# Kernel optimization log

Measured on AMD Instinct MI355X. Metric: run time of the kernel, lower is better.

Reference implementation:

```python
import jax, jax.numpy as jnp
import numpy as np

IN_CH, C_M, C_N = 512, 512, 128
B, H, W = 16, 56, 56


def setup_inputs() -> dict:
    key = jax.random.key(0)
    ks = jax.random.split(key, 7)
    s = 1.0 / np.sqrt(IN_CH)
    return {
        "x": jax.random.normal(ks[0], (B, IN_CH, H, W), dtype=jnp.float32),
        "wA": jax.random.uniform(ks[1], (C_M, IN_CH), jnp.float32, -s, s),
        "bA": jax.random.uniform(ks[2], (C_M,), jnp.float32, -s, s),
        "wB": jax.random.uniform(ks[3], (C_N, IN_CH), jnp.float32, -s, s),
        "bB": jax.random.uniform(ks[4], (C_N,), jnp.float32, -s, s),
        "wV": jax.random.uniform(ks[5], (C_N, IN_CH), jnp.float32, -s, s),
        "bV": jax.random.uniform(ks[6], (C_N,), jnp.float32, -s, s),
        "K": 1,
    }


def reference(x, wA, bA, wB, bB, wV, bV, K):
    b, c, h, w = x.shape
    c_m, c_n = wA.shape[0], wB.shape[0]
    batch = b // K
    hw = h * w
    N = K * hw
    # 1x1 convs == channel-wise matmuls
    A = jnp.einsum('bchw,mc->bmhw', x, wA) + bA[None, :, None, None]
    Bf = jnp.einsum('bchw,nc->bnhw', x, wB) + bB[None, :, None, None]
    Vf = jnp.einsum('bchw,nc->bnhw', x, wV) + bV[None, :, None, None]
    # (batch, c_m, K*h*w)
    tmpA = A.reshape(batch, K, c_m, hw).transpose(0, 2, 1, 3).reshape(batch, c_m, N)
    # softmax over the spatial dim N (torch Softmax() on 2D -> dim=1)
    tmpB = Bf.reshape(batch, K, c_n, hw).transpose(0, 2, 1, 3).reshape(batch, c_n, N)
    attB = jax.nn.softmax(tmpB, axis=-1).transpose(0, 2, 1)  # (batch, N, c_n)
    # softmax over channel dim c_n
    tmpV = Vf.reshape(batch, K, c_n, hw).transpose(0, 1, 3, 2).reshape(batch, N, c_n)
    attV = jax.nn.softmax(tmpV, axis=-1).transpose(0, 2, 1)  # (batch, c_n, N)
    G = jnp.matmul(tmpA, attB)   # (batch, c_m, c_n) global descriptors
    Z = jnp.matmul(G, attV)      # (batch, c_m, N) distribute
    Z = Z.reshape(batch, c_m, K, hw).transpose(0, 2, 1, 3).reshape(b, c_m, h, w)
    return Z
```

## Files before the change

kernel.cpp:

```cpp
#include <hip/hip_runtime.h>
#include <hip/hip_bf16.h>

#define BATCH 16
#define CIN   512
#define HW    3136
#define CM    512
#define CN    128

typedef short short8 __attribute__((ext_vector_type(8)));
typedef float f32x4  __attribute__((ext_vector_type(4)));

#define MFMA(a,b,c) __builtin_amdgcn_mfma_f32_16x16x32_bf16((a),(b),(c),0,0,0)

__device__ __forceinline__ void cvt_store8(__bf16* dst, const float* src) {
  const f32x4 a = *(const f32x4*)src;
  const f32x4 b = *(const f32x4*)(src + 4);
  __attribute__((aligned(16))) __bf16 t[8];
  t[0] = (__bf16)a[0]; t[1] = (__bf16)a[1]; t[2] = (__bf16)a[2]; t[3] = (__bf16)a[3];
  t[4] = (__bf16)b[0]; t[5] = (__bf16)b[1]; t[6] = (__bf16)b[2]; t[7] = (__bf16)b[3];
  *(uint4*)dst = *(uint4*)t;
}

__device__ __forceinline__ void load_lds16(const void* g, void* l) {
  __builtin_amdgcn_global_load_lds(
      (const __attribute__((address_space(1))) unsigned int*)g,
      (__attribute__((address_space(3))) unsigned int*)l, 16, 0, 0);
}

__global__ __launch_bounds__(256) void prep_w_kernel(
    const float* __restrict__ wB, const float* __restrict__ wV,
    __bf16* __restrict__ Wimg)
{
  const int k0  = blockIdx.x >> 2;
  const int row = (blockIdx.x & 3) * 64 + (threadIdx.x >> 2);
  const int c0  = (threadIdx.x & 3) * 16;
  const float* src = (row < 128) ? (wB + (size_t)row * CIN)
                                 : (wV + (size_t)(row - 128) * CIN);
  src += k0 * 64 + c0;
  __bf16* dst = Wimg + (size_t)k0 * 18432 + row * 72 + c0;
  cvt_store8(dst, src);
  cvt_store8(dst + 8, src + 8);
}

__global__ __launch_bounds__(256) void conv_bv_kernel(
    const float* __restrict__ x,
    const __bf16* __restrict__ Wimg,
    const float* __restrict__ bB, const float* __restrict__ bV,
    __bf16* __restrict__ BVB, __bf16* __restrict__ attVT,
    float* __restrict__ bsum)
{
  const int s0  = blockIdx.x * 64;
  const int b   = blockIdx.y;
  const int tid = threadIdx.x;
  const int lane = tid & 63, w = tid >> 6;
  const int l15  = lane & 15, q = lane >> 4;

  __shared__ __attribute__((aligned(16))) char smem[46080];
  __bf16* Wt = (__bf16*)smem;
  __bf16* Xt = (__bf16*)(smem + 36864);
  __bf16* T  = (__bf16*)smem;
  __shared__ float Vm[2][64];
  __shared__ float Vs[2][64];

  f32x4 acc[4][4] = {};
  const float* xb = x + (size_t)b*CIN*HW + s0;
  const int colg = tid & 7;
  const int cl = 2*(tid >> 3);
  const int xoff = ((cl >> 3) ^ colg)*8 + (cl & 7);

  f32x4 pa0, pa1, pb0, pb1;
  {
    const float* r0 = xb + (size_t)cl*HW + colg*8;
    const float* r1 = r0 + HW;
    pa0 = *(const f32x4*)r0; pa1 = *(const f32x4*)(r0 + 4);
    pb0 = *(const f32x4*)r1; pb1 = *(const f32x4*)(r1 + 4);
  }

  for (int k0 = 0; k0 < CIN; k0 += 64) {
    {
      float va[8] = {pa0[0],pa0[1],pa0[2],pa0[3],pa1[0],pa1[1],pa1[2],pa1[3]};
      float vb[8] = {pb0[0],pb0[1],pb0[2],pb0[3],pb1[0],pb1[1],pb1[2],pb1[3]};
      #pragma unroll
      for (int j = 0; j < 8; ++j) {
        int s = colg*8 + j;
        __attribute__((aligned(4))) __bf16 pairv[2] = { (__bf16)va[j], (__bf16)vb[j] };
        *(unsigned int*)&Xt[s*72 + xoff] = *(unsigned int*)pairv;
      }
    }
    {
      const char* wsrc = (const char*)Wimg + (size_t)(k0 >> 6)*36864 + tid*16;
      char* wdst = (char*)Wt + tid*16;
      #pragma unroll
      for (int i = 0; i < 9; ++i)
        load_lds16(wsrc + i*4096, wdst + i*4096);
    }
    if (k0 + 64 < CIN) {
      const float* r0 = xb + (size_t)(k0 + 64 + cl)*HW + colg*8;
      const float* r1 = r0 + HW;
      pa0 = *(const f32x4*)r0; pa1 = *(const f32x4*)(r0 + 4);
      pb0 = *(const f32x4*)r1; pb1 = *(const f32x4*)(r1 + 4);
    }
    __syncthreads();
    #pragma unroll
    for (int kk = 0; kk < 2; ++kk) {
      short8 a[4], bb[4];
      #pragma unroll
      for (int mi = 0; mi < 4; ++mi)
        a[mi] = *(short8*)&Wt[(w*64 + mi*16 + l15)*72 + kk*32 + q*8];
      #pragma unroll
      for (int si = 0; si < 4; ++si) {
        int s = si*16 + l15;
        int oct = (kk*4 + q) ^ (si*2 + (l15 >> 3));
        bb[si] = *(short8*)&Xt[s*72 + oct*8];
      }
      #pragma unroll
      for (int mi = 0; mi < 4; ++mi)
        #pragma unroll
        for (int si = 0; si < 4; ++si)
          acc[mi][si] = MFMA(a[mi], bb[si], acc[mi][si]);
    }
    __syncthreads();
  }

  float bias[4][4];
  #pragma unroll
  for (int mi = 0; mi < 4; ++mi)
    #pragma unroll
    for (int r = 0; r < 4; ++r) {
      int nch = w*64 + mi*16 + q*4 + r;
      bias[mi][r] = (nch < CN) ? bB[nch] : bV[nch - CN];
    }

  if (w < 2) {
    const size_t outb = (size_t)b * CN * HW;
    float psum[4][4] = {};
    #pragma unroll
    for (int mi = 0; mi < 4; ++mi)
      #pragma unroll
      for (int si = 0; si < 4; ++si) {
        int s = s0 + si*16 + l15;
        #pragma unroll
        for (int r = 0; r < 4; ++r) {
          int nch = w*64 + mi*16 + q*4 + r;
          __bf16 bv = (__bf16)(acc[mi][si][r] + bias[mi][r]);
          BVB[outb + (size_t)nch*HW + s] = bv;
          psum[mi][r] += __expf((float)bv);
        }
      }
    #pragma unroll
    for (int mi = 0; mi < 4; ++mi)
      #pragma unroll
      for (int r = 0; r < 4; ++r) {
        float v = psum[mi][r];
        v += __shfl_xor(v, 1); v += __shfl_xor(v, 2);
        v += __shfl_xor(v, 4); v += __shfl_xor(v, 8);
        if (l15 == 0) {
          int nch = w*64 + mi*16 + q*4 + r;
          atomicAdd(&bsum[b*CN + nch], v);
        }
      }
  } else {
    #pragma unroll
    for (int si = 0; si < 4; ++si) {
      float m = -1e30f;
      #pragma unroll
      for (int mi = 0; mi < 4; ++mi)
        #pragma unroll
        for (int r = 0; r < 4; ++r)
          m = fmaxf(m, acc[mi][si][r] + bias[mi][r]);
      m = fmaxf(m, __shfl_xor(m, 16));
      m = fmaxf(m, __shfl_xor(m, 32));
      if (q == 0) Vm[w-2][si*16 + l15] = m;
    }
  }
  __syncthreads();
  if (w >= 2) {
    #pragma unroll
    for (int si = 0; si < 4; ++si) {
      int idx = si*16 + l15;
      float ms = fmaxf(Vm[0][idx], Vm[1][idx]);
      float ssum = 0.f;
      #pragma unroll
      for (int mi = 0; mi < 4; ++mi)
        #pragma unroll
        for (int r = 0; r < 4; ++r) {
          float e = __expf(acc[mi][si][r] + bias[mi][r] - ms);
          acc[mi][si][r] = e;
          ssum += e;
        }
      ssum += __shfl_xor(ssum, 16);
      ssum += __shfl_xor(ssum, 32);
      if (q == 0) Vs[w-2][idx] = ssum;
    }
  }
  __syncthreads();
  if (w >= 2) {
    #pragma unroll
    for (int si = 0; si < 4; ++si) {
      int idx = si*16 + l15;
      float inv = 1.0f / (Vs[0][idx] + Vs[1][idx]);
      #pragma unroll
      for (int mi = 0; mi < 4; ++mi)
        #pragma unroll
        for (int r = 0; r < 4; ++r) {
          int j = (w-2)*64 + mi*16 + q*4 + r;
          T[idx*136 + j] = (__bf16)(acc[mi][si][r] * inv);
        }
    }
  }
  __syncthreads();
  __bf16* dst = attVT + ((size_t)b*HW + s0)*CN;
  #pragma unroll
  for (int k = 0; k < 4; ++k) {
    int chunk = tid + 256*k;
    int row = chunk >> 4, oct = chunk & 15;
    *(uint4*)&dst[(size_t)row*CN + oct*8] = *(uint4*)&T[row*136 + oct*8];
  }
}

__global__ __launch_bounds__(256) void h_gemm_kernel(
    const float* __restrict__ x, const __bf16* __restrict__ BVB,
    const float* __restrict__ bsum, float* __restrict__ H)
{
  const int c0 = blockIdx.x * 128, b = blockIdx.y, kc = blockIdx.z;
  const int tid = threadIdx.x, lane = tid & 63, w = tid >> 6;
  const int l15 = lane & 15, q = lane >> 4;

  __shared__ __attribute__((aligned(16))) __bf16 At[128*72];
  __shared__ __attribute__((aligned(16))) __bf16 Bt[128*72];
  f32x4 acc[8][2] = {};

  const float* xb = x + ((size_t)b*CIN + c0)*HW;
  const __bf16* ab = BVB + (size_t)b*CN*HW;
  const float* bsb = bsum + b*CN;
  const int colg = tid & 7, row0 = tid >> 3;

  float irow[4];
  #pragma unroll
  for (int p = 0; p < 4; ++p) irow[p] = 1.0f / bsb[row0 + 32*p];

  for (int ki = 0; ki < 7; ++ki) {
    int k0 = kc*448 + ki*64;
    #pragma unroll
    for (int p = 0; p < 4; ++p) {
      int row = row0 + 32*p;
      cvt_store8(&At[row*72 + colg*8], xb + (size_t)row*HW + k0 + colg*8);
    }
    #pragma unroll
    for (int p = 0; p < 4; ++p) {
      int row = row0 + 32*p;
      uint4 rawv = *(const uint4*)(ab + (size_t)row*HW + k0 + colg*8);
      const __bf16* v = (const __bf16*)&rawv;
      __attribute__((aligned(16))) __bf16 t[8];
      #pragma unroll
      for (int j = 0; j < 8; ++j)
        t[j] = (__bf16)(__expf((float)v[j]) * irow[p]);
      *(uint4*)&Bt[row*72 + colg*8] = *(uint4*)t;
    }
    __syncthreads();
    #pragma unroll
    for (int kk = 0; kk < 2; ++kk) {
      short8 a[8], bb[2];
      #pragma unroll
      for (int mi = 0; mi < 8; ++mi)
        a[mi] = *(short8*)&At[(mi*16 + l15)*72 + kk*32 + q*8];
      #pragma unroll
      for (int ni = 0; ni < 2; ++ni)
        bb[ni] = *(short8*)&Bt[(w*32 + ni*16 + l15)*72 + kk*32 + q*8];
      #pragma unroll
      for (int mi = 0; mi < 8; ++mi)
        #pragma unroll
        for (int ni = 0; ni < 2; ++ni)
          acc[mi][ni] = MFMA(a[mi], bb[ni], acc[mi][ni]);
    }
    __syncthreads();
  }

  float* Hb = H + (size_t)b*CIN*CN;
  #pragma unroll
  for (int mi = 0; mi < 8; ++mi)
    #pragma unroll
    for (int ni = 0; ni < 2; ++ni)
      #pragma unroll
      for (int r = 0; r < 4; ++r) {
        int c = c0 + mi*16 + q*4 + r;
        int n = w*32 + ni*16 + l15;
        atomicAdd(&Hb[c*CN + n], acc[mi][ni][r]);
      }
}

__global__ __launch_bounds__(256) void g_gemm_kernel(
    const float* __restrict__ wA, const float* __restrict__ bA,
    const float* __restrict__ H, __bf16* __restrict__ G)
{
  const int m0 = blockIdx.x * 64, b = blockIdx.y;
  const int tid = threadIdx.x, lane = tid & 63, w = tid >> 6;
  const int l15 = lane & 15, q = lane >> 4;

  __shared__ __attribute__((aligned(16))) __bf16 At[64*72];
  __shared__ __attribute__((aligned(16))) __bf16 Bt[128*72];
  f32x4 acc[4][2] = {};

  const float* Hb = H + (size_t)b*CIN*CN;
  const int colg = tid & 7, row0 = tid >> 3;
  const int nn = tid & 127, gh = tid >> 7;

  for (int k0 = 0; k0 < CIN; k0 += 64) {
    #pragma unroll
    for (int p = 0; p < 2; ++p) {
      int row = row0 + 32*p;
      cvt_store8(&At[row*72 + colg*8], wA + (size_t)(m0+row)*CIN + k0 + colg*8);
    }
    #pragma unroll
    for (int p = 0; p < 4; ++p) {
      int g = gh + 2*p;
      __attribute__((aligned(16))) __bf16 tmp[8];
      #pragma unroll
      for (int j = 0; j < 8; ++j)
        tmp[j] = (__bf16)Hb[(size_t)(k0 + g*8 + j)*CN + nn];
      *(uint4*)&Bt[nn*72 + g*8] = *(uint4*)tmp;
    }
    __syncthreads();
    #pragma unroll
    for (int kk = 0; kk < 2; ++kk) {
      short8 a[4], bb[2];
      #pragma unroll
      for (int mi = 0; mi < 4; ++mi)
        a[mi] = *(short8*)&At[(mi*16 + l15)*72 + kk*32 + q*8];
      #pragma unroll
      for (int ni = 0; ni < 2; ++ni)
        bb[ni] = *(short8*)&Bt[(w*32 + ni*16 + l15)*72 + kk*32 + q*8];
      #pragma unroll
      for (int mi = 0; mi < 4; ++mi)
        #pragma unroll
        for (int ni = 0; ni < 2; ++ni)
          acc[mi][ni] = MFMA(a[mi], bb[ni], acc[mi][ni]);
    }
    __syncthreads();
  }

  #pragma unroll
  for (int mi = 0; mi < 4; ++mi)
    #pragma unroll
    for (int ni = 0; ni < 2; ++ni)
      #pragma unroll
      for (int r = 0; r < 4; ++r) {
        int m = m0 + mi*16 + q*4 + r;
        int n = w*32 + ni*16 + l15;
        G[((size_t)b*CM + m)*CN + n] = (__bf16)(acc[mi][ni][r] + bA[m]);
      }
}

__global__ __launch_bounds__(256) void z_gemm_kernel(
    const __bf16* __restrict__ G, const __bf16* __restrict__ attVT,
    float* __restrict__ out)
{
  const int m0 = blockIdx.x * 128, s0 = blockIdx.y * 64, b = blockIdx.z;
  const int tid = threadIdx.x, lane = tid & 63, w = tid >> 6;
  const int l15 = lane & 15, q = lane >> 4;

  __shared__ __attribute__((aligned(16))) __bf16 At[128*136];
  __shared__ __attribute__((aligned(16))) __bf16 Bt[64*136];

  const __bf16* Gb = G + ((size_t)b*CM + m0)*CN;
  const __bf16* Vb = attVT + ((size_t)b*HW + s0)*CN;
  const int g = tid & 15, r0 = tid >> 4;
  #pragma unroll
  for (int p = 0; p < 8; ++p) {
    int row = r0 + 16*p;
    *(uint4*)&At[row*136 + g*8] = *(const uint4*)(Gb + (size_t)row*CN + g*8);
  }
  #pragma unroll
  for (int p = 0; p < 4; ++p) {
    int row = r0 + 16*p;
    *(uint4*)&Bt[row*136 + g*8] = *(const uint4*)(Vb + (size_t)row*CN + g*8);
  }
  __syncthreads();

  f32x4 acc[8] = {};
  #pragma unroll
  for (int kk = 0; kk < 4; ++kk) {
    short8 bb = *(short8*)&Bt[(w*16 + l15)*136 + kk*32 + q*8];
    #pragma unroll
    for (int mi = 0; mi < 8; ++mi) {
      short8 a = *(short8*)&At[(mi*16 + l15)*136 + kk*32 + q*8];
      acc[mi] = MFMA(a, bb, acc[mi]);
    }
  }

  const int s = s0 + w*16 + l15;
  #pragma unroll
  for (int mi = 0; mi < 8; ++mi)
    #pragma unroll
    for (int r = 0; r < 4; ++r) {
      int m = m0 + mi*16 + q*4 + r;
      out[((size_t)b*CM + m)*HW + s] = acc[mi][r];
    }
}

extern "C" void kernel_launch(void* const* d_in, const int* in_sizes, int n_in,
                              void* d_out, int out_size, void* d_ws, size_t ws_size,
                              hipStream_t stream)
{
  (void)in_sizes; (void)n_in; (void)out_size; (void)ws_size;
  const float* x  = (const float*)d_in[0];
  const float* wA = (const float*)d_in[1];
  const float* bA = (const float*)d_in[2];
  const float* wB = (const float*)d_in[3];
  const float* bB = (const float*)d_in[4];
  const float* wV = (const float*)d_in[5];
  const float* bV = (const float*)d_in[6];
  float* out = (float*)d_out;

  char* ws = (char*)d_ws;
  const size_t szBVB   = (size_t)BATCH*CN*HW*2;
  const size_t szAttVT = (size_t)BATCH*HW*CN*2;
  const size_t szH     = (size_t)BATCH*CIN*CN*4;
  const size_t szBsum  = (size_t)BATCH*CN*4;
  const size_t szG     = (size_t)BATCH*CM*CN*2;

  char* p = ws;
  __bf16* BVB   = (__bf16*)p; p += szBVB;
  __bf16* attVT = (__bf16*)p; p += szAttVT;
  float*  H     = (float*)p;  p += szH;
  float*  bsum  = (float*)p;  p += szBsum;
  __bf16* G     = (__bf16*)p; p += szG;
  __bf16* Wimg  = (__bf16*)p;

  hipMemsetAsync(H, 0, szH + szBsum, stream);
  prep_w_kernel <<<dim3(32),      256, 0, stream>>>(wB, wV, Wimg);
  conv_bv_kernel<<<dim3(49,16),   256, 0, stream>>>(x, Wimg, bB, bV, BVB, attVT, bsum);
  h_gemm_kernel <<<dim3(4,16,7),  256, 0, stream>>>(x, BVB, bsum, H);
  g_gemm_kernel <<<dim3(8,16),    256, 0, stream>>>(wA, bA, H, G);
  z_gemm_kernel <<<dim3(4,49,16), 256, 0, stream>>>(G, attVT, out);
}
```

Before: 283.8 us.

## Prefetch next tile in h_gemm and load z_gemm fragments directly from global

In h_gemm, the global loads of x and the exp'd B tile for the next k-step are issued into registers before the barrier and MMA work, so memory latency overlaps compute. z_gemm drops LDS staging entirely: each wave loads its MFMA fragments straight from global memory with double-buffered registers. It now computes a 64x64 tile per wave with 256 rows per block, halving the grid. This raises register pressure and relies on L2 to absorb the repeated fragment reads that LDS sharing used to cover.

```diff
diff --git a/kernel.cpp b/kernel.cpp
--- a/kernel.cpp
+++ b/kernel.cpp
@@ -15,6 +15,13 @@
 __device__ __forceinline__ void cvt_store8(__bf16* dst, const float* src) {
   const f32x4 a = *(const f32x4*)src;
   const f32x4 b = *(const f32x4*)(src + 4);
+  __attribute__((aligned(16))) __bf16 t[8];
+  t[0] = (__bf16)a[0]; t[1] = (__bf16)a[1]; t[2] = (__bf16)a[2]; t[3] = (__bf16)a[3];
+  t[4] = (__bf16)b[0]; t[5] = (__bf16)b[1]; t[6] = (__bf16)b[2]; t[7] = (__bf16)b[3];
+  *(uint4*)dst = *(uint4*)t;
+}
+
+__device__ __forceinline__ void cvt_store8v(__bf16* dst, f32x4 a, f32x4 b) {
   __attribute__((aligned(16))) __bf16 t[8];
   t[0] = (__bf16)a[0]; t[1] = (__bf16)a[1]; t[2] = (__bf16)a[2]; t[3] = (__bf16)a[3];
   t[4] = (__bf16)b[0]; t[5] = (__bf16)b[1]; t[6] = (__bf16)b[2]; t[7] = (__bf16)b[3];
@@ -239,24 +246,36 @@
   #pragma unroll
   for (int p = 0; p < 4; ++p) irow[p] = 1.0f / bsb[row0 + 32*p];
 
+  f32x4 px[4][2];
+  uint4 pB[4];
+#define HLOAD(K0) do { \
+    _Pragma("unroll") \
+    for (int p = 0; p < 4; ++p) { \
+      const float* s_ = xb + (size_t)(row0 + 32*p)*HW + (K0) + colg*8; \
+      px[p][0] = *(const f32x4*)s_; px[p][1] = *(const f32x4*)(s_ + 4); \
+    } \
+    _Pragma("unroll") \
+    for (int p = 0; p < 4; ++p) \
+      pB[p] = *(const uint4*)(ab + (size_t)(row0 + 32*p)*HW + (K0) + colg*8); \
+  } while(0)
+
+  const int kbase = kc * 448;
+  HLOAD(kbase);
+
   for (int ki = 0; ki < 7; ++ki) {
-    int k0 = kc*448 + ki*64;
+    #pragma unroll
+    for (int p = 0; p < 4; ++p)
+      cvt_store8v(&At[(row0 + 32*p)*72 + colg*8], px[p][0], px[p][1]);
     #pragma unroll
     for (int p = 0; p < 4; ++p) {
-      int row = row0 + 32*p;
-      cvt_store8(&At[row*72 + colg*8], xb + (size_t)row*HW + k0 + colg*8);
-    }
-    #pragma unroll
-    for (int p = 0; p < 4; ++p) {
-      int row = row0 + 32*p;
-      uint4 rawv = *(const uint4*)(ab + (size_t)row*HW + k0 + colg*8);
-      const __bf16* v = (const __bf16*)&rawv;
+      const __bf16* v = (const __bf16*)&pB[p];
       __attribute__((aligned(16))) __bf16 t[8];
       #pragma unroll
       for (int j = 0; j < 8; ++j)
         t[j] = (__bf16)(__expf((float)v[j]) * irow[p]);
-      *(uint4*)&Bt[row*72 + colg*8] = *(uint4*)t;
-    }
+      *(uint4*)&Bt[(row0 + 32*p)*72 + colg*8] = *(uint4*)t;
+    }
+    if (ki < 6) HLOAD(kbase + (ki + 1)*64);
     __syncthreads();
     #pragma unroll
     for (int kk = 0; kk < 2; ++kk) {
@@ -275,6 +294,7 @@
     }
     __syncthreads();
   }
+#undef HLOAD
 
   float* Hb = H + (size_t)b*CIN*CN;
   #pragma unroll
@@ -355,46 +375,45 @@
     const __bf16* __restrict__ G, const __bf16* __restrict__ attVT,
     float* __restrict__ out)
 {
-  const int m0 = blockIdx.x * 128, s0 = blockIdx.y * 64, b = blockIdx.z;
+  const int s0 = blockIdx.y * 64, b = blockIdx.z;
   const int tid = threadIdx.x, lane = tid & 63, w = tid >> 6;
   const int l15 = lane & 15, q = lane >> 4;
-
-  __shared__ __attribute__((aligned(16))) __bf16 At[128*136];
-  __shared__ __attribute__((aligned(16))) __bf16 Bt[64*136];
-
-  const __bf16* Gb = G + ((size_t)b*CM + m0)*CN;
-  const __bf16* Vb = attVT + ((size_t)b*HW + s0)*CN;
-  const int g = tid & 15, r0 = tid >> 4;
-  #pragma unroll
-  for (int p = 0; p < 8; ++p) {
-    int row = r0 + 16*p;
-    *(uint4*)&At[row*136 + g*8] = *(const uint4*)(Gb + (size_t)row*CN + g*8);
-  }
-  #pragma unroll
-  for (int p = 0; p < 4; ++p) {
-    int row = r0 + 16*p;
-    *(uint4*)&Bt[row*136 + g*8] = *(const uint4*)(Vb + (size_t)row*CN + g*8);
-  }
-  __syncthreads();
-
-  f32x4 acc[8] = {};
+  const int m0 = blockIdx.x * 256 + w * 64;
+
+  const __bf16* Ga = G + ((size_t)(b*CM + m0 + l15))*CN + q*8;
+  const __bf16* Va = attVT + ((size_t)(b*HW + s0 + l15))*CN + q*8;
+
+  f32x4 acc[4][4] = {};
+  short8 a[2][4], bb[2][4];
+#define ZLOAD(P, KK) do { \
+    _Pragma("unroll") for (int mi_ = 0; mi_ < 4; ++mi_) \
+      a[P][mi_] = *(const short8*)(Ga + (size_t)mi_*16*CN + (KK)*32); \
+    _Pragma("unroll") for (int si_ = 0; si_ < 4; ++si_) \
+      bb[P][si_] = *(const short8*)(Va + (size_t)si_*16*CN + (KK)*32); } while(0)
+
+  ZLOAD(0, 0);
   #pragma unroll
   for (int kk = 0; kk < 4; ++kk) {
-    short8 bb = *(short8*)&Bt[(w*16 + l15)*136 + kk*32 + q*8];
-    #pragma unroll
-    for (int mi = 0; mi < 8; ++mi) {
-      short8 a = *(short8*)&At[(mi*16 + l15)*136 + kk*32 + q*8];
-      acc[mi] = MFMA(a, bb, acc[mi]);
-    }
-  }
-
-  const int s = s0 + w*16 + l15;
-  #pragma unroll
-  for (int mi = 0; mi < 8; ++mi)
-    #pragma unroll
-    for (int r = 0; r < 4; ++r) {
-      int m = m0 + mi*16 + q*4 + r;
-      out[((size_t)b*CM + m)*HW + s] = acc[mi][r];
+    const int p = kk & 1;
+    if (kk < 3) ZLOAD(p^1, kk+1);
+    #pragma unroll
+    for (int mi = 0; mi < 4; ++mi)
+      #pragma unroll
+      for (int si = 0; si < 4; ++si)
+        acc[mi][si] = MFMA(a[p][mi], bb[p][si], acc[mi][si]);
+  }
+#undef ZLOAD
+
+  #pragma unroll
+  for (int mi = 0; mi < 4; ++mi)
+    #pragma unroll
+    for (int si = 0; si < 4; ++si) {
+      const int s = s0 + si*16 + l15;
+      #pragma unroll
+      for (int r = 0; r < 4; ++r) {
+        int m = m0 + mi*16 + q*4 + r;
+        out[((size_t)b*CM + m)*HW + s] = acc[mi][si][r];
+      }
     }
 }
 
@@ -432,5 +451,5 @@
   conv_bv_kernel<<<dim3(49,16),   256, 0, stream>>>(x, Wimg, bB, bV, BVB, attVT, bsum);
   h_gemm_kernel <<<dim3(4,16,7),  256, 0, stream>>>(x, BVB, bsum, H);
   g_gemm_kernel <<<dim3(8,16),    256, 0, stream>>>(wA, bA, H, G);
-  z_gemm_kernel <<<dim3(4,49,16), 256, 0, stream>>>(G, attVT, out);
-}
+  z_gemm_kernel <<<dim3(2,49,16), 256, 0, stream>>>(G, attVT, out);
+}
```

Measured after the change: 288.6 us. Within noise of the previous version (+1.7%).

## Store exp(B) directly, defer softmax normalization to G GEMM, prefetch H-GEMM tiles

Applied to the files above, without the earlier changes.

The conv kernel now writes exp of the B logits instead of the raw logits, so the H GEMM no longer computes exp or multiplies by the inverse row sum while loading tiles. The 1/sum softmax normalization is moved algebraically into the G GEMM, where it scales each column of H as it is loaded. The H GEMM also gains register prefetching of the next k-tile of x and expB, overlapping global loads with MFMA work. Storing exp in bf16 changes rounding slightly and the prefetch adds register pressure.

```diff
diff --git a/kernel.cpp b/kernel.cpp
--- a/kernel.cpp
+++ b/kernel.cpp
@@ -15,6 +15,13 @@
 __device__ __forceinline__ void cvt_store8(__bf16* dst, const float* src) {
   const f32x4 a = *(const f32x4*)src;
   const f32x4 b = *(const f32x4*)(src + 4);
+  __attribute__((aligned(16))) __bf16 t[8];
+  t[0] = (__bf16)a[0]; t[1] = (__bf16)a[1]; t[2] = (__bf16)a[2]; t[3] = (__bf16)a[3];
+  t[4] = (__bf16)b[0]; t[5] = (__bf16)b[1]; t[6] = (__bf16)b[2]; t[7] = (__bf16)b[3];
+  *(uint4*)dst = *(uint4*)t;
+}
+
+__device__ __forceinline__ void cvt_store8v(__bf16* dst, f32x4 a, f32x4 b) {
   __attribute__((aligned(16))) __bf16 t[8];
   t[0] = (__bf16)a[0]; t[1] = (__bf16)a[1]; t[2] = (__bf16)a[2]; t[3] = (__bf16)a[3];
   t[4] = (__bf16)b[0]; t[5] = (__bf16)b[1]; t[6] = (__bf16)b[2]; t[7] = (__bf16)b[3];
@@ -46,7 +53,7 @@
     const float* __restrict__ x,
     const __bf16* __restrict__ Wimg,
     const float* __restrict__ bB, const float* __restrict__ bV,
-    __bf16* __restrict__ BVB, __bf16* __restrict__ attVT,
+    __bf16* __restrict__ expB, __bf16* __restrict__ attVT,
     float* __restrict__ bsum)
 {
   const int s0  = blockIdx.x * 64;
@@ -143,8 +150,9 @@
         for (int r = 0; r < 4; ++r) {
           int nch = w*64 + mi*16 + q*4 + r;
           __bf16 bv = (__bf16)(acc[mi][si][r] + bias[mi][r]);
-          BVB[outb + (size_t)nch*HW + s] = bv;
-          psum[mi][r] += __expf((float)bv);
+          float e = __expf((float)bv);
+          expB[outb + (size_t)nch*HW + s] = (__bf16)e;
+          psum[mi][r] += e;
         }
       }
     #pragma unroll
@@ -219,8 +227,8 @@
 }
 
 __global__ __launch_bounds__(256) void h_gemm_kernel(
-    const float* __restrict__ x, const __bf16* __restrict__ BVB,
-    const float* __restrict__ bsum, float* __restrict__ H)
+    const float* __restrict__ x, const __bf16* __restrict__ expB,
+    float* __restrict__ H)
 {
   const int c0 = blockIdx.x * 128, b = blockIdx.y, kc = blockIdx.z;
   const int tid = threadIdx.x, lane = tid & 63, w = tid >> 6;
@@ -231,32 +239,33 @@
   f32x4 acc[8][2] = {};
 
   const float* xb = x + ((size_t)b*CIN + c0)*HW;
-  const __bf16* ab = BVB + (size_t)b*CN*HW;
-  const float* bsb = bsum + b*CN;
+  const __bf16* ab = expB + (size_t)b*CN*HW;
   const int colg = tid & 7, row0 = tid >> 3;
 
-  float irow[4];
-  #pragma unroll
-  for (int p = 0; p < 4; ++p) irow[p] = 1.0f / bsb[row0 + 32*p];
+  f32x4 px[4][2];
+  uint4 pB[4];
+#define HLOAD(K0) do { \
+    _Pragma("unroll") \
+    for (int p = 0; p < 4; ++p) { \
+      const float* s_ = xb + (size_t)(row0 + 32*p)*HW + (K0) + colg*8; \
+      px[p][0] = *(const f32x4*)s_; px[p][1] = *(const f32x4*)(s_ + 4); \
+    } \
+    _Pragma("unroll") \
+    for (int p = 0; p < 4; ++p) \
+      pB[p] = *(const uint4*)(ab + (size_t)(row0 + 32*p)*HW + (K0) + colg*8); \
+  } while(0)
+
+  const int kbase = kc * 448;
+  HLOAD(kbase);
 
   for (int ki = 0; ki < 7; ++ki) {
-    int k0 = kc*448 + ki*64;
-    #pragma unroll
-    for (int p = 0; p < 4; ++p) {
-      int row = row0 + 32*p;
-      cvt_store8(&At[row*72 + colg*8], xb + (size_t)row*HW + k0 + colg*8);
-    }
-    #pragma unroll
-    for (int p = 0; p < 4; ++p) {
-      int row = row0 + 32*p;
-      uint4 rawv = *(const uint4*)(ab + (size_t)row*HW + k0 + colg*8);
-      const __bf16* v = (const __bf16*)&rawv;
-      __attribute__((aligned(16))) __bf16 t[8];
-      #pragma unroll
-      for (int j = 0; j < 8; ++j)
-        t[j] = (__bf16)(__expf((float)v[j]) * irow[p]);
-      *(uint4*)&Bt[row*72 + colg*8] = *(uint4*)t;
-    }
+    #pragma unroll
+    for (int p = 0; p < 4; ++p)
+      cvt_store8v(&At[(row0 + 32*p)*72 + colg*8], px[p][0], px[p][1]);
+    #pragma unroll
+    for (int p = 0; p < 4; ++p)
+      *(uint4*)&Bt[(row0 + 32*p)*72 + colg*8] = pB[p];
+    if (ki < 6) HLOAD(kbase + (ki + 1)*64);
     __syncthreads();
     #pragma unroll
     for (int kk = 0; kk < 2; ++kk) {
@@ -275,6 +284,7 @@
     }
     __syncthreads();
   }
+#undef HLOAD
 
   float* Hb = H + (size_t)b*CIN*CN;
   #pragma unroll
@@ -291,7 +301,8 @@
 
 __global__ __launch_bounds__(256) void g_gemm_kernel(
     const float* __restrict__ wA, const float* __restrict__ bA,
-    const float* __restrict__ H, __bf16* __restrict__ G)
+    const float* __restrict__ H, const float* __restrict__ bsum,
+    __bf16* __restrict__ G)
 {
   const int m0 = blockIdx.x * 64, b = blockIdx.y;
   const int tid = threadIdx.x, lane = tid & 63, w = tid >> 6;
@@ -304,6 +315,7 @@
   const float* Hb = H + (size_t)b*CIN*CN;
   const int colg = tid & 7, row0 = tid >> 3;
   const int nn = tid & 127, gh = tid >> 7;
+  const float inv = 1.0f / bsum[b*CN + nn];
 
   for (int k0 = 0; k0 < CIN; k0 += 64) {
     #pragma unroll
@@ -317,7 +329,7 @@
       __attribute__((aligned(16))) __bf16 tmp[8];
       #pragma unroll
       for (int j = 0; j < 8; ++j)
-        tmp[j] = (__bf16)Hb[(size_t)(k0 + g*8 + j)*CN + nn];
+        tmp[j] = (__bf16)(Hb[(size_t)(k0 + g*8 + j)*CN + nn] * inv);
       *(uint4*)&Bt[nn*72 + g*8] = *(uint4*)tmp;
     }
     __syncthreads();
@@ -420,7 +432,7 @@
   const size_t szG     = (size_t)BATCH*CM*CN*2;
 
   char* p = ws;
-  __bf16* BVB   = (__bf16*)p; p += szBVB;
+  __bf16* expB  = (__bf16*)p; p += szBVB;
   __bf16* attVT = (__bf16*)p; p += szAttVT;
   float*  H     = (float*)p;  p += szH;
   float*  bsum  = (float*)p;  p += szBsum;
@@ -429,8 +441,8 @@
 
   hipMemsetAsync(H, 0, szH + szBsum, stream);
   prep_w_kernel <<<dim3(32),      256, 0, stream>>>(wB, wV, Wimg);
-  conv_bv_kernel<<<dim3(49,16),   256, 0, stream>>>(x, Wimg, bB, bV, BVB, attVT, bsum);
-  h_gemm_kernel <<<dim3(4,16,7),  256, 0, stream>>>(x, BVB, bsum, H);
-  g_gemm_kernel <<<dim3(8,16),    256, 0, stream>>>(wA, bA, H, G);
+  conv_bv_kernel<<<dim3(49,16),   256, 0, stream>>>(x, Wimg, bB, bV, expB, attVT, bsum);
+  h_gemm_kernel <<<dim3(4,16,7),  256, 0, stream>>>(x, expB, H);
+  g_gemm_kernel <<<dim3(8,16),    256, 0, stream>>>(wA, bA, H, bsum, G);
   z_gemm_kernel <<<dim3(4,49,16), 256, 0, stream>>>(G, attVT, out);
 }
```

New measurement: 286.3 us. No clear change (+0.9%).
